# Performance work log

Hardware: AMD Instinct MI355X
Metric: run time of the kernel (lower is better)

## Reference

```python
import jax, jax.numpy as jnp
import numpy as np

D_MODEL = 1024
N_HEADS = 16
D_HEAD = D_MODEL // N_HEADS
EPS = 1e-6


def setup_inputs() -> dict:
    key = jax.random.key(0)
    ks = jax.random.split(key, 11)
    N, L, S = 4, 4096, 4096
    scale = 1.0 / np.sqrt(D_MODEL)
    inp = {
        "queries": jax.random.normal(ks[0], (N, L, D_MODEL), jnp.float32),
        "keys": jax.random.normal(ks[1], (N, S, D_MODEL), jnp.float32),
        "values": jax.random.normal(ks[2], (N, S, D_MODEL), jnp.float32),
        "Wq": jax.random.normal(ks[3], (D_MODEL, D_MODEL), jnp.float32) * scale,
        "bq": jnp.zeros((D_MODEL,), jnp.float32),
        "Wk": jax.random.normal(ks[4], (D_MODEL, D_MODEL), jnp.float32) * scale,
        "bk": jnp.zeros((D_MODEL,), jnp.float32),
        "Wv": jax.random.normal(ks[5], (D_MODEL, D_MODEL), jnp.float32) * scale,
        "bv": jnp.zeros((D_MODEL,), jnp.float32),
        "Wo": jax.random.normal(ks[6], (D_MODEL, D_MODEL), jnp.float32) * scale,
        "bo": jnp.zeros((D_MODEL,), jnp.float32),
    }
    return inp


def reference(queries, keys, values, Wq, bq, Wk, bk, Wv, bv, Wo, bo):
    N, L, _ = queries.shape
    S = keys.shape[1]
    H, Dh = N_HEADS, D_HEAD
    # projections (torch Linear: x @ W.T + b)
    q = (queries @ Wq.T + bq).reshape(N, L, H, Dh)
    k = (keys @ Wk.T + bk).reshape(N, S, H, Dh)
    v = (values @ Wv.T + bv).reshape(N, S, H, Dh)
    # elu+1 feature map
    Q = jax.nn.elu(q) + 1.0
    K = jax.nn.elu(k) + 1.0
    # KV summary: [N,H,Dv,Dh]
    KV = jnp.einsum('nshd,nshm->nhmd', K, v)
    # normalizer: [N,L,H]
    Z = 1.0 / (jnp.einsum('nlhd,nhd->nlh', Q, K.sum(axis=1)) + EPS)
    # output per head: [N,L,H,Dv]
    V = jnp.einsum('nlhd,nhmd,nlh->nlhm', Q, KV, Z)
    out = V.reshape(N, L, H * Dh) @ Wo.T + bo
    return out
```

## Files before the change

### kernel.cpp

```cpp
#include <hip/hip_runtime.h>
#include <hip/hip_bf16.h>

typedef __attribute__((ext_vector_type(8))) short short8;
typedef __attribute__((ext_vector_type(4))) short short4v;
typedef __attribute__((ext_vector_type(4))) float f32x4;

#define MFMA16(a, b, c) __builtin_amdgcn_mfma_f32_16x16x32_bf16(a, b, c, 0, 0, 0)

__device__ __forceinline__ unsigned short f2bf(float f) {
    unsigned int u = __float_as_uint(f);
    unsigned int r = u + 0x7fffu + ((u >> 16) & 1u);
    return (unsigned short)(r >> 16);
}
__device__ __forceinline__ float bf2f(unsigned short h) {
    return __uint_as_float(((unsigned int)h) << 16);
}
__device__ __forceinline__ unsigned int pk2(float lo, float hi) {
    return (unsigned int)f2bf(lo) | ((unsigned int)f2bf(hi) << 16);
}

__device__ __forceinline__ void async16(const void* g, void* l) {
    __builtin_amdgcn_global_load_lds(
        (const __attribute__((address_space(1))) unsigned int*)g,
        (__attribute__((address_space(3))) unsigned int*)l, 16, 0, 0);
}

#define S_BARRIER() asm volatile("s_barrier" ::: "memory")
#define SCHED_FENCE() __builtin_amdgcn_sched_barrier(0)

__global__ __launch_bounds__(256) void cvt_all(const float* __restrict__ q,
                                               const float* __restrict__ k,
                                               const float* __restrict__ v,
                                               const float* __restrict__ Wq,
                                               const float* __restrict__ Wk,
                                               const float* __restrict__ Wv,
                                               const float* __restrict__ Wo,
                                               unsigned short* __restrict__ qb,
                                               unsigned short* __restrict__ kb,
                                               unsigned short* __restrict__ vb,
                                               unsigned short* __restrict__ Wqb,
                                               unsigned short* __restrict__ Wkb,
                                               unsigned short* __restrict__ Wvb,
                                               unsigned short* __restrict__ Wob) {
    int b = blockIdx.x;
    const float* in;
    unsigned short* out;
    int lb, nb, n8;
    if (b < 6144) {
        int s = b >> 11;
        lb = b & 2047; nb = 2048; n8 = 2097152;
        in = s == 0 ? q : s == 1 ? k : v;
        out = s == 0 ? qb : s == 1 ? kb : vb;
    } else {
        int s = b - 6144;
        int w = s >> 7;
        lb = s & 127; nb = 128; n8 = 131072;
        in = w == 0 ? Wq : w == 1 ? Wk : w == 2 ? Wv : Wo;
        out = w == 0 ? Wqb : w == 1 ? Wkb : w == 2 ? Wvb : Wob;
    }
    for (int i = lb * 256 + threadIdx.x; i < n8; i += nb * 256) {
        float4 v0 = reinterpret_cast<const float4*>(in)[2 * i];
        float4 v1 = reinterpret_cast<const float4*>(in)[2 * i + 1];
        uint4 p;
        p.x = pk2(v0.x, v0.y); p.y = pk2(v0.z, v0.w);
        p.z = pk2(v1.x, v1.y); p.w = pk2(v1.z, v1.w);
        reinterpret_cast<uint4*>(out)[i] = p;
    }
}

__device__ __forceinline__ void gemm_body(const unsigned short* __restrict__ A,
                                          const unsigned short* __restrict__ B,
                                          const float* __restrict__ bias,
                                          void* __restrict__ out,
                                          int mode, char* lds, int bid) {
    const int tid = threadIdx.x;
    const int lane = tid & 63, wid = tid >> 6;
    const int wr = wid >> 2, wc = wid & 3;
    const int lr = lane & 15, lg = lane >> 4;

    const int swz = (bid & 7) * 32 + (bid >> 3);
    const int bm = swz >> 2, bn = swz & 3;
    const long row0 = (long)bm * 256;
    const long col0 = (long)bn * 256;

    const unsigned short* srcA[2];
    const unsigned short* srcB[2];
    int dstOff[2];
#pragma unroll
    for (int g = 0; g < 2; ++g) {
        int s = g * 512 + tid;
        int pr = s >> 3;
        int dc = (s & 7) ^ (pr & 7);
        srcA[g] = A + (row0 + (pr & 63) + 128 * (pr >> 6)) * 1024 + dc * 8;
        srcB[g] = B + (col0 + pr) * 1024 + dc * 8;
        dstOff[g] = s * 16;
    }

#define STG_AQ(BB, Q, KT) do {                                                  \
        async16(srcA[0] + (Q) * 65536 + (KT) * 64,                              \
                lds + (BB) * 65536 + (Q) * 16384 + dstOff[0]);                  \
        async16(srcA[1] + (Q) * 65536 + (KT) * 64,                              \
                lds + (BB) * 65536 + (Q) * 16384 + dstOff[1]); } while (0)
#define STG_BH(BB, H, KT) do {                                                  \
        async16(srcB[0] + (H) * 131072 + (KT) * 64,                             \
                lds + (BB) * 65536 + 32768 + (H) * 16384 + dstOff[0]);          \
        async16(srcB[1] + (H) * 131072 + (KT) * 64,                             \
                lds + (BB) * 65536 + 32768 + (H) * 16384 + dstOff[1]); } while (0)

    const int ch0 = (((0 * 4 + lg) ^ (lr & 7)) << 4);
    const int ch1 = (((1 * 4 + lg) ^ (lr & 7)) << 4);
    const int aB0 = (64 * wr + lr) * 128 + ch0;
    const int aB1 = (64 * wr + lr) * 128 + ch1;
    const int bB0 = 32768 + (wc >> 1) * 16384 + ((wc & 1) * 64 + lr) * 128 + ch0;
    const int bB1 = 32768 + (wc >> 1) * 16384 + ((wc & 1) * 64 + lr) * 128 + ch1;

    f32x4 acc[8][4] = {};
    short8 b0[4], b1[4];

#define GATE4() do { asm volatile("s_waitcnt vmcnt(4)" ::: "memory"); SCHED_FENCE(); } while (0)
#define GATE0() do { asm volatile("s_waitcnt vmcnt(0)" ::: "memory"); SCHED_FENCE(); } while (0)
#define MFMA_BLOCK(MB, BV) do {                                                 \
        asm volatile("s_waitcnt lgkmcnt(0)" ::: "memory");                      \
        SCHED_FENCE();                                                          \
        __builtin_amdgcn_s_setprio(1);                                          \
        _Pragma("unroll") for (int m = 0; m < 4; ++m)                           \
            _Pragma("unroll") for (int n = 0; n < 4; ++n)                       \
                acc[(MB) + m][n] = MFMA16(a[m], BV[n], acc[(MB) + m][n]);       \
        __builtin_amdgcn_s_setprio(0);                                          \
        SCHED_FENCE();                                                          \
        S_BARRIER(); } while (0)
#define LOAD_A(BUFB, ABASE, Q) do {                                             \
        _Pragma("unroll") for (int m = 0; m < 4; ++m)                           \
            a[m] = *(const short8*)(lds + (BUFB) + (Q) * 16384 + (ABASE) + m * 2048); } while (0)
#define LOAD_B(BUFB, BBASE, BV) do {                                            \
        _Pragma("unroll") for (int n = 0; n < 4; ++n)                           \
            BV[n] = *(const short8*)(lds + (BUFB) + (BBASE) + n * 2048); } while (0)

    STG_AQ(0, 0, 0); STG_BH(0, 0, 0); STG_BH(0, 1, 0); STG_AQ(0, 1, 0);
    STG_AQ(1, 0, 1); STG_BH(1, 0, 1);
    GATE4();
    S_BARRIER();

#pragma unroll 1
    for (int t = 0; t < 7; ++t) {
        const int ktA = 2 * t + 1, ktB = 2 * t + 2, ktC = 2 * t + 3;
        { short8 a[4]; LOAD_B(0, bB0, b0); LOAD_A(0, aB0, 0); STG_BH(1, 1, ktA); MFMA_BLOCK(0, b0); }
        { short8 a[4]; LOAD_B(0, bB1, b1); LOAD_A(0, aB1, 0); STG_AQ(1, 1, ktA); MFMA_BLOCK(0, b1); }
        { short8 a[4]; LOAD_A(0, aB0, 1); STG_AQ(0, 0, ktB); MFMA_BLOCK(4, b0); }
        { short8 a[4]; LOAD_A(0, aB1, 1); STG_BH(0, 0, ktB); GATE4(); MFMA_BLOCK(4, b1); }
        { short8 a[4]; LOAD_B(65536, bB0, b0); LOAD_A(65536, aB0, 0); STG_BH(0, 1, ktB); MFMA_BLOCK(0, b0); }
        { short8 a[4]; LOAD_B(65536, bB1, b1); LOAD_A(65536, aB1, 0); STG_AQ(0, 1, ktB); MFMA_BLOCK(0, b1); }
        { short8 a[4]; LOAD_A(65536, aB0, 1); STG_AQ(1, 0, ktC); MFMA_BLOCK(4, b0); }
        { short8 a[4]; LOAD_A(65536, aB1, 1); STG_BH(1, 0, ktC); GATE4(); MFMA_BLOCK(4, b1); }
    }
    {
        { short8 a[4]; LOAD_B(0, bB0, b0); LOAD_A(0, aB0, 0); STG_BH(1, 1, 15); MFMA_BLOCK(0, b0); }
        { short8 a[4]; LOAD_B(0, bB1, b1); LOAD_A(0, aB1, 0); STG_AQ(1, 1, 15); MFMA_BLOCK(0, b1); }
        { short8 a[4]; LOAD_A(0, aB0, 1); MFMA_BLOCK(4, b0); }
        { short8 a[4]; LOAD_A(0, aB1, 1); GATE0(); MFMA_BLOCK(4, b1); }
        { short8 a[4]; LOAD_B(65536, bB0, b0); LOAD_A(65536, aB0, 0); MFMA_BLOCK(0, b0); }
        { short8 a[4]; LOAD_B(65536, bB1, b1); LOAD_A(65536, aB1, 0); MFMA_BLOCK(0, b1); }
        { short8 a[4]; LOAD_A(65536, aB0, 1); MFMA_BLOCK(4, b0); }
        { short8 a[4]; LOAD_A(65536, aB1, 1); MFMA_BLOCK(4, b1); }
    }
#undef STG_AQ
#undef STG_BH
#undef GATE4
#undef GATE0
#undef MFMA_BLOCK
#undef LOAD_A
#undef LOAD_B

    const int r4 = lg * 4;
    if (mode == 0 || mode == 3) {
        char* ep = lds + wid * 4608;
#pragma unroll
        for (int m = 0; m < 8; ++m) {
#pragma unroll
            for (int n = 0; n < 4; ++n) {
                float bcol = bias[col0 + wc * 64 + n * 16 + lr];
#pragma unroll
                for (int j = 0; j < 4; ++j) {
                    float v = acc[m][n][j] + bcol;
                    if (mode == 0) v = v > 0.f ? v + 1.f : __expf(v);
                    *(float*)(ep + (((lg * 4 + j) * 68) + n * 16 + lr) * 4) = v;
                }
            }
            asm volatile("s_waitcnt lgkmcnt(0)" ::: "memory");
            SCHED_FENCE();
            long R0b = row0 + wr * 128 + m * 16;
            if (mode == 0) {
                unsigned short* O = (unsigned short*)out;
#pragma unroll
                for (int i = 0; i < 2; ++i) {
                    int r = i * 8 + (lane >> 3), c8 = (lane & 7) * 8;
                    float4 u0 = *(const float4*)(ep + (r * 68 + c8) * 4);
                    float4 u1 = *(const float4*)(ep + (r * 68 + c8 + 4) * 4);
                    uint4 w;
                    w.x = pk2(u0.x, u0.y); w.y = pk2(u0.z, u0.w);
                    w.z = pk2(u1.x, u1.y); w.w = pk2(u1.z, u1.w);
                    *(uint4*)(O + (R0b + r) * 1024 + col0 + wc * 64 + c8) = w;
                }
            } else {
                float* O = (float*)out;
#pragma unroll
                for (int i = 0; i < 4; ++i) {
                    int r = i * 4 + (lane >> 4), c4 = (lane & 15) * 4;
                    float4 u = *(const float4*)(ep + (r * 68 + c4) * 4);
                    *(float4*)(O + (R0b + r) * 1024 + col0 + wc * 64 + c4) = u;
                }
            }
            asm volatile("s_waitcnt lgkmcnt(0)" ::: "memory");
            SCHED_FENCE();
        }
    } else {
#pragma unroll
        for (int m = 0; m < 8; ++m) {
#pragma unroll
            for (int n = 0; n < 4; ++n) {
                long col = col0 + wc * 64 + n * 16 + lr;
                float bcol = bias[col];
                long R0 = row0 + wr * 128 + m * 16 + r4;
                unsigned short* O = (unsigned short*)out;
                long nb = R0 >> 12;
                long s = R0 & 4095;
                short4v pack;
#pragma unroll
                for (int j = 0; j < 4; ++j) {
                    float v = acc[m][n][j] + bcol;
                    if (mode == 1) v = v > 0.f ? v + 1.f : __expf(v);
                    pack[j] = (short)f2bf(v);
                }
                *(short4v*)(O + ((nb << 10) + col) * 4096 + s) = pack;
            }
        }
    }
}

__global__ __launch_bounds__(512, 1) void proj_gemm(const unsigned short* __restrict__ qb,
                                                    const unsigned short* __restrict__ kb,
                                                    const unsigned short* __restrict__ vb,
                                                    const unsigned short* __restrict__ Wqb,
                                                    const unsigned short* __restrict__ Wkb,
                                                    const unsigned short* __restrict__ Wvb,
                                                    const float* __restrict__ bq,
                                                    const float* __restrict__ bk,
                                                    const float* __restrict__ bv,
                                                    unsigned short* __restrict__ Qm,
                                                    unsigned short* __restrict__ Kt,
                                                    unsigned short* __restrict__ vT) {
    __shared__ __align__(16) char lds[131072];
    int seg = blockIdx.x >> 8;
    int bid = blockIdx.x & 255;
    const unsigned short* A = seg == 0 ? qb : seg == 1 ? kb : vb;
    const unsigned short* B = seg == 0 ? Wqb : seg == 1 ? Wkb : Wvb;
    const float* bias = seg == 0 ? bq : seg == 1 ? bk : bv;
    void* out = seg == 0 ? (void*)Qm : seg == 1 ? (void*)Kt : (void*)vT;
    gemm_body(A, B, bias, out, seg, lds, bid);
}

__global__ __launch_bounds__(512, 1) void out_gemm(const unsigned short* __restrict__ Vbuf,
                                                   const unsigned short* __restrict__ Wob,
                                                   const float* __restrict__ bo,
                                                   float* __restrict__ out) {
    __shared__ __align__(16) char lds[131072];
    gemm_body(Vbuf, Wob, bo, out, 3, lds, blockIdx.x);
}

__global__ __launch_bounds__(256) void kv_kernel(const unsigned short* __restrict__ Kt,
                                                 const unsigned short* __restrict__ vT,
                                                 float* __restrict__ KV,
                                                 float* __restrict__ Ksum) {
    int b = blockIdx.x;
    int sc = b & 7, h = (b >> 3) & 15, n = b >> 7;
    const int tid = threadIdx.x, lane = tid & 63, wave = tid >> 6;
    long base = ((long)(n * 1024 + h * 64)) * 4096 + sc * 512;
    const unsigned short* Kp = Kt + base;
    const unsigned short* Vp = vT + base;
    const int lr = lane & 15, lk = (lane >> 4) * 8;

    f32x4 acc[4] = {};
    float ksa[4] = {0.f, 0.f, 0.f, 0.f};
    for (int s0 = 0; s0 < 512; s0 += 32) {
        short8 a = *(const short8*)(Vp + (long)(wave * 16 + lr) * 4096 + s0 + lk);
#pragma unroll
        for (int d4 = 0; d4 < 4; ++d4) {
            short8 bb = *(const short8*)(Kp + (long)(d4 * 16 + lr) * 4096 + s0 + lk);
            acc[d4] = MFMA16(a, bb, acc[d4]);
            if (wave == 0) {
                float t = 0.f;
#pragma unroll
                for (int e = 0; e < 8; ++e) t += bf2f((unsigned short)bb[e]);
                ksa[d4] += t;
            }
        }
    }
    float* KVb = KV + (long)(n * 16 + h) * 4096;
#pragma unroll
    for (int d4 = 0; d4 < 4; ++d4)
#pragma unroll
        for (int j = 0; j < 4; ++j) {
            int m = wave * 16 + (lane >> 4) * 4 + j;
            int d = d4 * 16 + lr;
            atomicAdd(KVb + m * 64 + d, acc[d4][j]);
        }
    if (wave == 0) {
#pragma unroll
        for (int d4 = 0; d4 < 4; ++d4) {
            float t = ksa[d4];
            t += __shfl_xor(t, 16, 64);
            t += __shfl_xor(t, 32, 64);
            if (lane < 16) atomicAdd(Ksum + n * 1024 + h * 64 + d4 * 16 + lane, t);
        }
    }
}

__global__ __launch_bounds__(256) void attn_kernel(const unsigned short* __restrict__ Qm,
                                                   const float* __restrict__ KV,
                                                   const float* __restrict__ Ksum,
                                                   unsigned short* __restrict__ Vbuf) {
    __shared__ unsigned short Qs[128 * 64];
    __shared__ unsigned short KVs[64 * 64];
    __shared__ float zin[128];
    __shared__ float ks[64];
    int b = blockIdx.x;
    int lc = b & 31, h = (b >> 5) & 15, n = b >> 9;
    int tid = threadIdx.x, lane = tid & 63, wave = tid >> 6;
    long l0 = (long)n * 4096 + lc * 128;

    const unsigned short* Qg = Qm + (l0 + (tid >> 3)) * 1024 + h * 64 + (tid & 7) * 8;
    char* QsB = (char*)Qs + (wave << 10);
#pragma unroll
    for (int it = 0; it < 4; ++it)
        async16(Qg + (long)it * 32 * 1024, QsB + it * 4096);

    const float* kvp = KV + (long)(n * 16 + h) * 4096;
    for (int i = tid * 4; i < 4096; i += 1024) {
        float4 v = *reinterpret_cast<const float4*>(kvp + i);
        short4v p;
        p[0] = (short)f2bf(v.x); p[1] = (short)f2bf(v.y);
        p[2] = (short)f2bf(v.z); p[3] = (short)f2bf(v.w);
        *(short4v*)(KVs + i) = p;
    }
    if (tid < 64) ks[tid] = Ksum[n * 1024 + h * 64 + tid];
    __syncthreads();

    {
        int row = tid >> 1, half = tid & 1;
        float den = 0.f;
        const unsigned short* qrow = Qs + row * 64 + half * 32;
#pragma unroll
        for (int d = 0; d < 32; ++d) den += bf2f(qrow[d]) * ks[half * 32 + d];
        den += __shfl_xor(den, 1, 64);
        if (half == 0) zin[row] = 1.0f / (den + 1e-6f);
    }
    __syncthreads();

    const int lr = lane & 15, lk = (lane >> 4) * 8;
    f32x4 acc[2][4] = {};
#pragma unroll
    for (int kk = 0; kk < 2; ++kk) {
        short8 a0 = *(const short8*)(Qs + (wave * 32 + lr) * 64 + kk * 32 + lk);
        short8 a1 = *(const short8*)(Qs + (wave * 32 + 16 + lr) * 64 + kk * 32 + lk);
#pragma unroll
        for (int nn = 0; nn < 4; ++nn) {
            short8 bb = *(const short8*)(KVs + (nn * 16 + lr) * 64 + kk * 32 + lk);
            acc[0][nn] = MFMA16(a0, bb, acc[0][nn]);
            acc[1][nn] = MFMA16(a1, bb, acc[1][nn]);
        }
    }

    {
        char* ep = (char*)Qs + wave * 4096;
#pragma unroll
        for (int mi = 0; mi < 2; ++mi) {
#pragma unroll
            for (int nn = 0; nn < 4; ++nn)
#pragma unroll
                for (int j = 0; j < 4; ++j) {
                    int rloc = (lane >> 4) * 4 + j;
                    float v = acc[mi][nn][j] * zin[wave * 32 + mi * 16 + rloc];
                    *(float*)(ep + (rloc * 64 + nn * 16 + lr) * 4) = v;
                }
            asm volatile("s_waitcnt lgkmcnt(0)" ::: "memory");
            SCHED_FENCE();
#pragma unroll
            for (int i = 0; i < 2; ++i) {
                int r = i * 8 + (lane >> 3), c8 = (lane & 7) * 8;
                float4 u0 = *(const float4*)(ep + (r * 64 + c8) * 4);
                float4 u1 = *(const float4*)(ep + (r * 64 + c8 + 4) * 4);
                uint4 w;
                w.x = pk2(u0.x, u0.y); w.y = pk2(u0.z, u0.w);
                w.z = pk2(u1.x, u1.y); w.w = pk2(u1.z, u1.w);
                *(uint4*)(Vbuf + (l0 + wave * 32 + mi * 16 + r) * 1024 + h * 64 + c8) = w;
            }
            asm volatile("s_waitcnt lgkmcnt(0)" ::: "memory");
            SCHED_FENCE();
        }
    }
}

extern "C" void kernel_launch(void* const* d_in, const int* in_sizes, int n_in,
                              void* d_out, int out_size, void* d_ws, size_t ws_size,
                              hipStream_t stream) {
    const float* queries = (const float*)d_in[0];
    const float* keys    = (const float*)d_in[1];
    const float* values  = (const float*)d_in[2];
    const float* Wq = (const float*)d_in[3];
    const float* bq = (const float*)d_in[4];
    const float* Wk = (const float*)d_in[5];
    const float* bk = (const float*)d_in[6];
    const float* Wv = (const float*)d_in[7];
    const float* bv = (const float*)d_in[8];
    const float* Wo = (const float*)d_in[9];
    const float* bo = (const float*)d_in[10];
    float* out = (float*)d_out;

    char* ws = (char*)d_ws;
    const size_t SZ = (size_t)16384 * 1024 * 2;
    const size_t WSZ = (size_t)1024 * 1024 * 2;
    unsigned short* qb  = (unsigned short*)(ws);
    unsigned short* kb  = (unsigned short*)(ws + SZ);
    unsigned short* vb  = (unsigned short*)(ws + 2 * SZ);
    unsigned short* Wqb = (unsigned short*)(ws + 3 * SZ);
    unsigned short* Wkb = (unsigned short*)(ws + 3 * SZ + WSZ);
    unsigned short* Wvb = (unsigned short*)(ws + 3 * SZ + 2 * WSZ);
    unsigned short* Wob = (unsigned short*)(ws + 3 * SZ + 3 * WSZ);
    unsigned short* Qm  = (unsigned short*)(ws + 3 * SZ + 4 * WSZ);
    unsigned short* Kt  = (unsigned short*)(ws + 4 * SZ + 4 * WSZ);
    unsigned short* vT  = (unsigned short*)(ws + 5 * SZ + 4 * WSZ);
    float* KVf = (float*)(ws + 6 * SZ + 4 * WSZ);
    float* Ksf = (float*)(ws + 6 * SZ + 4 * WSZ + 1048576);
    unsigned short* Vbuf = qb;

    hipMemsetAsync(KVf, 0, 1048576 + 16384, stream);

    cvt_all<<<6656, 256, 0, stream>>>(queries, keys, values, Wq, Wk, Wv, Wo,
                                      qb, kb, vb, Wqb, Wkb, Wvb, Wob);

    proj_gemm<<<768, 512, 0, stream>>>(qb, kb, vb, Wqb, Wkb, Wvb, bq, bk, bv, Qm, Kt, vT);

    kv_kernel<<<512, 256, 0, stream>>>(Kt, vT, KVf, Ksf);
    attn_kernel<<<2048, 256, 0, stream>>>(Qm, KVf, Ksf, Vbuf);

    out_gemm<<<256, 512, 0, stream>>>(Vbuf, Wob, bo, out);
}
```

Before: 254.4 us.

## Double-buffer LDS fragment registers to overlap ds_reads with MFMA phases

Restructures the GEMM main loop so that LDS reads for the next MFMA phase are issued into alternate register sets (ax/ay, b0/b1) before the current phase's MFMAs run. Partial lgkmcnt waits replace full drains, so LDS read latency is hidden behind matrix math. The vmcnt gates are retuned to the new ordering of async global-to-LDS stages. This raises register pressure and depends on the barrier and wait counts staying correct so no read races a buffer being refilled.

```diff
diff --git a/kernel.cpp b/kernel.cpp
--- a/kernel.cpp
+++ b/kernel.cpp
@@ -107,69 +107,111 @@
         async16(srcB[1] + (H) * 131072 + (KT) * 64,                             \
                 lds + (BB) * 65536 + 32768 + (H) * 16384 + dstOff[1]); } while (0)
 
-    const int ch0 = (((0 * 4 + lg) ^ (lr & 7)) << 4);
-    const int ch1 = (((1 * 4 + lg) ^ (lr & 7)) << 4);
-    const int aB0 = (64 * wr + lr) * 128 + ch0;
-    const int aB1 = (64 * wr + lr) * 128 + ch1;
-    const int bB0 = 32768 + (wc >> 1) * 16384 + ((wc & 1) * 64 + lr) * 128 + ch0;
-    const int bB1 = 32768 + (wc >> 1) * 16384 + ((wc & 1) * 64 + lr) * 128 + ch1;
+    const int ch0 = ((lg ^ (lr & 7)) << 4);
+    const int ch1 = (((4 + lg) ^ (lr & 7)) << 4);
+    const int aBASE = (64 * wr + lr) * 128;
+    const int bBASE = 32768 + (wc >> 1) * 16384 + ((wc & 1) * 64 + lr) * 128;
 
     f32x4 acc[8][4] = {};
-    short8 b0[4], b1[4];
-
-#define GATE4() do { asm volatile("s_waitcnt vmcnt(4)" ::: "memory"); SCHED_FENCE(); } while (0)
+    short8 ax[4], ay[4], b0[4], b1[4];
+
+#define LD_A(DST, BB, Q, CH) do {                                               \
+        _Pragma("unroll") for (int m = 0; m < 4; ++m)                           \
+            DST[m] = *(const short8*)(lds + (BB) + (Q) * 16384 + aBASE + (CH) + m * 2048); } while (0)
+#define LD_B(DST, BB, CH) do {                                                  \
+        _Pragma("unroll") for (int n = 0; n < 4; ++n)                           \
+            DST[n] = *(const short8*)(lds + (BB) + bBASE + (CH) + n * 2048); } while (0)
+#define GATE2() do { asm volatile("s_waitcnt vmcnt(2)" ::: "memory"); SCHED_FENCE(); } while (0)
 #define GATE0() do { asm volatile("s_waitcnt vmcnt(0)" ::: "memory"); SCHED_FENCE(); } while (0)
-#define MFMA_BLOCK(MB, BV) do {                                                 \
-        asm volatile("s_waitcnt lgkmcnt(0)" ::: "memory");                      \
+#define PHASE(WN, MB, AV, BV) do {                                              \
+        asm volatile("s_waitcnt lgkmcnt(" #WN ")" ::: "memory");                \
         SCHED_FENCE();                                                          \
         __builtin_amdgcn_s_setprio(1);                                          \
         _Pragma("unroll") for (int m = 0; m < 4; ++m)                           \
             _Pragma("unroll") for (int n = 0; n < 4; ++n)                       \
-                acc[(MB) + m][n] = MFMA16(a[m], BV[n], acc[(MB) + m][n]);       \
+                acc[(MB) + m][n] = MFMA16(AV[m], BV[n], acc[(MB) + m][n]);      \
         __builtin_amdgcn_s_setprio(0);                                          \
         SCHED_FENCE();                                                          \
         S_BARRIER(); } while (0)
-#define LOAD_A(BUFB, ABASE, Q) do {                                             \
-        _Pragma("unroll") for (int m = 0; m < 4; ++m)                           \
-            a[m] = *(const short8*)(lds + (BUFB) + (Q) * 16384 + (ABASE) + m * 2048); } while (0)
-#define LOAD_B(BUFB, BBASE, BV) do {                                            \
-        _Pragma("unroll") for (int n = 0; n < 4; ++n)                           \
-            BV[n] = *(const short8*)(lds + (BUFB) + (BBASE) + n * 2048); } while (0)
 
     STG_AQ(0, 0, 0); STG_BH(0, 0, 0); STG_BH(0, 1, 0); STG_AQ(0, 1, 0);
     STG_AQ(1, 0, 1); STG_BH(1, 0, 1);
-    GATE4();
+    asm volatile("s_waitcnt vmcnt(4)" ::: "memory");
+    SCHED_FENCE();
     S_BARRIER();
+    LD_A(ax, 0, 0, ch0); LD_B(b0, 0, ch0);
+    SCHED_FENCE();
 
 #pragma unroll 1
     for (int t = 0; t < 7; ++t) {
         const int ktA = 2 * t + 1, ktB = 2 * t + 2, ktC = 2 * t + 3;
-        { short8 a[4]; LOAD_B(0, bB0, b0); LOAD_A(0, aB0, 0); STG_BH(1, 1, ktA); MFMA_BLOCK(0, b0); }
-        { short8 a[4]; LOAD_B(0, bB1, b1); LOAD_A(0, aB1, 0); STG_AQ(1, 1, ktA); MFMA_BLOCK(0, b1); }
-        { short8 a[4]; LOAD_A(0, aB0, 1); STG_AQ(0, 0, ktB); MFMA_BLOCK(4, b0); }
-        { short8 a[4]; LOAD_A(0, aB1, 1); STG_BH(0, 0, ktB); GATE4(); MFMA_BLOCK(4, b1); }
-        { short8 a[4]; LOAD_B(65536, bB0, b0); LOAD_A(65536, aB0, 0); STG_BH(0, 1, ktB); MFMA_BLOCK(0, b0); }
-        { short8 a[4]; LOAD_B(65536, bB1, b1); LOAD_A(65536, aB1, 0); STG_AQ(0, 1, ktB); MFMA_BLOCK(0, b1); }
-        { short8 a[4]; LOAD_A(65536, aB0, 1); STG_AQ(1, 0, ktC); MFMA_BLOCK(4, b0); }
-        { short8 a[4]; LOAD_A(65536, aB1, 1); STG_BH(1, 0, ktC); GATE4(); MFMA_BLOCK(4, b1); }
+        {
+            LD_A(ay, 0, 0, ch1); LD_B(b1, 0, ch1); SCHED_FENCE();
+            STG_BH(1, 1, ktA);
+            PHASE(8, 0, ax, b0);
+        }
+        {
+            LD_A(ax, 0, 1, ch0); SCHED_FENCE();
+            STG_AQ(1, 1, ktA);
+            PHASE(4, 0, ay, b1);
+        }
+        {
+            LD_A(ay, 0, 1, ch1); SCHED_FENCE();
+            STG_AQ(0, 0, ktB);
+            GATE2();
+            PHASE(4, 4, ax, b0);
+        }
+        {
+            LD_A(ax, 65536, 0, ch0); LD_B(b0, 65536, ch0); SCHED_FENCE();
+            STG_BH(0, 0, ktB);
+            PHASE(8, 4, ay, b1);
+        }
+        {
+            LD_A(ay, 65536, 0, ch1); LD_B(b1, 65536, ch1); SCHED_FENCE();
+            STG_BH(0, 1, ktB);
+            PHASE(8, 0, ax, b0);
+        }
+        {
+            LD_A(ax, 65536, 1, ch0); SCHED_FENCE();
+            STG_AQ(0, 1, ktB);
+            PHASE(4, 0, ay, b1);
+        }
+        {
+            LD_A(ay, 65536, 1, ch1); SCHED_FENCE();
+            STG_AQ(1, 0, ktC);
+            GATE2();
+            PHASE(4, 4, ax, b0);
+        }
+        {
+            LD_A(ax, 0, 0, ch0); LD_B(b0, 0, ch0); SCHED_FENCE();
+            STG_BH(1, 0, ktC);
+            PHASE(8, 4, ay, b1);
+        }
     }
     {
-        { short8 a[4]; LOAD_B(0, bB0, b0); LOAD_A(0, aB0, 0); STG_BH(1, 1, 15); MFMA_BLOCK(0, b0); }
-        { short8 a[4]; LOAD_B(0, bB1, b1); LOAD_A(0, aB1, 0); STG_AQ(1, 1, 15); MFMA_BLOCK(0, b1); }
-        { short8 a[4]; LOAD_A(0, aB0, 1); MFMA_BLOCK(4, b0); }
-        { short8 a[4]; LOAD_A(0, aB1, 1); GATE0(); MFMA_BLOCK(4, b1); }
-        { short8 a[4]; LOAD_B(65536, bB0, b0); LOAD_A(65536, aB0, 0); MFMA_BLOCK(0, b0); }
-        { short8 a[4]; LOAD_B(65536, bB1, b1); LOAD_A(65536, aB1, 0); MFMA_BLOCK(0, b1); }
-        { short8 a[4]; LOAD_A(65536, aB0, 1); MFMA_BLOCK(4, b0); }
-        { short8 a[4]; LOAD_A(65536, aB1, 1); MFMA_BLOCK(4, b1); }
+        { LD_A(ay, 0, 0, ch1); LD_B(b1, 0, ch1); SCHED_FENCE();
+          STG_BH(1, 1, 15); PHASE(8, 0, ax, b0); }
+        { LD_A(ax, 0, 1, ch0); SCHED_FENCE();
+          STG_AQ(1, 1, 15); PHASE(4, 0, ay, b1); }
+        { LD_A(ay, 0, 1, ch1); SCHED_FENCE();
+          GATE0(); PHASE(4, 4, ax, b0); }
+        { LD_A(ax, 65536, 0, ch0); LD_B(b0, 65536, ch0); SCHED_FENCE();
+          PHASE(8, 4, ay, b1); }
+        { LD_A(ay, 65536, 0, ch1); LD_B(b1, 65536, ch1); SCHED_FENCE();
+          PHASE(8, 0, ax, b0); }
+        { LD_A(ax, 65536, 1, ch0); SCHED_FENCE();
+          PHASE(4, 0, ay, b1); }
+        { LD_A(ay, 65536, 1, ch1); SCHED_FENCE();
+          PHASE(4, 4, ax, b0); }
+        { PHASE(0, 4, ay, b1); }
     }
 #undef STG_AQ
 #undef STG_BH
-#undef GATE4
+#undef LD_A
+#undef LD_B
+#undef GATE2
 #undef GATE0
-#undef MFMA_BLOCK
-#undef LOAD_A
-#undef LOAD_B
+#undef PHASE
 
     const int r4 = lg * 4;
     if (mode == 0 || mode == 3) {
```

Result: slower. 261.1 us (+2.6%).

## Restructure GEMM main loop into fat phases with whole-tile double buffering

Applied to the files above, without the earlier changes.

Replaces the eight fine-grained MFMA blocks per iteration, with their staggered quarter-tile async stages and vmcnt(4) gates, with four larger phases. Each phase loads all eight A fragments and four B fragments for one k-half and issues 32 MFMAs. A full next tile is staged into the other buffer during the first phase and waited on with vmcnt(0) in the second. The aim is fewer barriers and a simpler schedule with more MFMA work between syncs. The cost is higher register pressure and coarser overlap, because the full wait can stall on global loads.

```diff
diff --git a/kernel.cpp b/kernel.cpp
--- a/kernel.cpp
+++ b/kernel.cpp
@@ -107,69 +107,56 @@
         async16(srcB[1] + (H) * 131072 + (KT) * 64,                             \
                 lds + (BB) * 65536 + 32768 + (H) * 16384 + dstOff[1]); } while (0)
 
-    const int ch0 = (((0 * 4 + lg) ^ (lr & 7)) << 4);
-    const int ch1 = (((1 * 4 + lg) ^ (lr & 7)) << 4);
-    const int aB0 = (64 * wr + lr) * 128 + ch0;
-    const int aB1 = (64 * wr + lr) * 128 + ch1;
-    const int bB0 = 32768 + (wc >> 1) * 16384 + ((wc & 1) * 64 + lr) * 128 + ch0;
-    const int bB1 = 32768 + (wc >> 1) * 16384 + ((wc & 1) * 64 + lr) * 128 + ch1;
+    const int ch0 = ((lg ^ (lr & 7)) << 4);
+    const int ch1 = (((4 + lg) ^ (lr & 7)) << 4);
+    const int aBASE = (64 * wr + lr) * 128;
+    const int bBASE = 32768 + (wc >> 1) * 16384 + ((wc & 1) * 64 + lr) * 128;
 
     f32x4 acc[8][4] = {};
-    short8 b0[4], b1[4];
-
-#define GATE4() do { asm volatile("s_waitcnt vmcnt(4)" ::: "memory"); SCHED_FENCE(); } while (0)
+
 #define GATE0() do { asm volatile("s_waitcnt vmcnt(0)" ::: "memory"); SCHED_FENCE(); } while (0)
-#define MFMA_BLOCK(MB, BV) do {                                                 \
+#define FAT_PHASE(BB, CH, STG_STMTS) do {                                       \
+        short8 a_[8], b_[4];                                                    \
+        _Pragma("unroll") for (int m = 0; m < 4; ++m)                           \
+            a_[m] = *(const short8*)(lds + (BB) + aBASE + (CH) + m * 2048);     \
+        _Pragma("unroll") for (int m = 0; m < 4; ++m)                           \
+            a_[4 + m] = *(const short8*)(lds + (BB) + 16384 + aBASE + (CH) + m * 2048); \
+        _Pragma("unroll") for (int n = 0; n < 4; ++n)                           \
+            b_[n] = *(const short8*)(lds + (BB) + bBASE + (CH) + n * 2048);     \
+        SCHED_FENCE();                                                          \
+        STG_STMTS;                                                              \
         asm volatile("s_waitcnt lgkmcnt(0)" ::: "memory");                      \
         SCHED_FENCE();                                                          \
         __builtin_amdgcn_s_setprio(1);                                          \
-        _Pragma("unroll") for (int m = 0; m < 4; ++m)                           \
+        _Pragma("unroll") for (int m = 0; m < 8; ++m)                           \
             _Pragma("unroll") for (int n = 0; n < 4; ++n)                       \
-                acc[(MB) + m][n] = MFMA16(a[m], BV[n], acc[(MB) + m][n]);       \
+                acc[m][n] = MFMA16(a_[m], b_[n], acc[m][n]);                    \
         __builtin_amdgcn_s_setprio(0);                                          \
         SCHED_FENCE();                                                          \
         S_BARRIER(); } while (0)
-#define LOAD_A(BUFB, ABASE, Q) do {                                             \
-        _Pragma("unroll") for (int m = 0; m < 4; ++m)                           \
-            a[m] = *(const short8*)(lds + (BUFB) + (Q) * 16384 + (ABASE) + m * 2048); } while (0)
-#define LOAD_B(BUFB, BBASE, BV) do {                                            \
-        _Pragma("unroll") for (int n = 0; n < 4; ++n)                           \
-            BV[n] = *(const short8*)(lds + (BUFB) + (BBASE) + n * 2048); } while (0)
-
-    STG_AQ(0, 0, 0); STG_BH(0, 0, 0); STG_BH(0, 1, 0); STG_AQ(0, 1, 0);
-    STG_AQ(1, 0, 1); STG_BH(1, 0, 1);
-    GATE4();
+
+    STG_AQ(0, 0, 0); STG_AQ(0, 1, 0); STG_BH(0, 0, 0); STG_BH(0, 1, 0);
+    GATE0();
     S_BARRIER();
 
 #pragma unroll 1
-    for (int t = 0; t < 7; ++t) {
-        const int ktA = 2 * t + 1, ktB = 2 * t + 2, ktC = 2 * t + 3;
-        { short8 a[4]; LOAD_B(0, bB0, b0); LOAD_A(0, aB0, 0); STG_BH(1, 1, ktA); MFMA_BLOCK(0, b0); }
-        { short8 a[4]; LOAD_B(0, bB1, b1); LOAD_A(0, aB1, 0); STG_AQ(1, 1, ktA); MFMA_BLOCK(0, b1); }
-        { short8 a[4]; LOAD_A(0, aB0, 1); STG_AQ(0, 0, ktB); MFMA_BLOCK(4, b0); }
-        { short8 a[4]; LOAD_A(0, aB1, 1); STG_BH(0, 0, ktB); GATE4(); MFMA_BLOCK(4, b1); }
-        { short8 a[4]; LOAD_B(65536, bB0, b0); LOAD_A(65536, aB0, 0); STG_BH(0, 1, ktB); MFMA_BLOCK(0, b0); }
-        { short8 a[4]; LOAD_B(65536, bB1, b1); LOAD_A(65536, aB1, 0); STG_AQ(0, 1, ktB); MFMA_BLOCK(0, b1); }
-        { short8 a[4]; LOAD_A(65536, aB0, 1); STG_AQ(1, 0, ktC); MFMA_BLOCK(4, b0); }
-        { short8 a[4]; LOAD_A(65536, aB1, 1); STG_BH(1, 0, ktC); GATE4(); MFMA_BLOCK(4, b1); }
-    }
-    {
-        { short8 a[4]; LOAD_B(0, bB0, b0); LOAD_A(0, aB0, 0); STG_BH(1, 1, 15); MFMA_BLOCK(0, b0); }
-        { short8 a[4]; LOAD_B(0, bB1, b1); LOAD_A(0, aB1, 0); STG_AQ(1, 1, 15); MFMA_BLOCK(0, b1); }
-        { short8 a[4]; LOAD_A(0, aB0, 1); MFMA_BLOCK(4, b0); }
-        { short8 a[4]; LOAD_A(0, aB1, 1); GATE0(); MFMA_BLOCK(4, b1); }
-        { short8 a[4]; LOAD_B(65536, bB0, b0); LOAD_A(65536, aB0, 0); MFMA_BLOCK(0, b0); }
-        { short8 a[4]; LOAD_B(65536, bB1, b1); LOAD_A(65536, aB1, 0); MFMA_BLOCK(0, b1); }
-        { short8 a[4]; LOAD_A(65536, aB0, 1); MFMA_BLOCK(4, b0); }
-        { short8 a[4]; LOAD_A(65536, aB1, 1); MFMA_BLOCK(4, b1); }
+    for (int t = 0; t < 8; ++t) {
+        const int kt1 = 2 * t + 1, kt2 = 2 * t + 2;
+        FAT_PHASE(0, ch0,
+                  { STG_AQ(1, 0, kt1); STG_AQ(1, 1, kt1); STG_BH(1, 0, kt1); STG_BH(1, 1, kt1); });
+        FAT_PHASE(0, ch1, { GATE0(); });
+        if (t < 7) {
+            FAT_PHASE(65536, ch0,
+                      { STG_AQ(0, 0, kt2); STG_AQ(0, 1, kt2); STG_BH(0, 0, kt2); STG_BH(0, 1, kt2); });
+        } else {
+            FAT_PHASE(65536, ch0, {});
+        }
+        FAT_PHASE(65536, ch1, { GATE0(); });
     }
 #undef STG_AQ
 #undef STG_BH
-#undef GATE4
 #undef GATE0
-#undef MFMA_BLOCK
-#undef LOAD_A
-#undef LOAD_B
+#undef FAT_PHASE
 
     const int r4 = lg * 4;
     if (mode == 0 || mode == 3) {
```

Result: slower. 747.4 us (+193.8%).
